# Kernel tuning notes

Hardware: AMD Instinct MI355X
Metric: run time of the kernel (lower is better)

Reference implementation:

```python
import jax, jax.numpy as jnp
import numpy as np

CH_J = 64      # number of output capsules
N_J = 32       # output capsule dim
R_NUM = 3      # routing iterations
B_ALPHAS = (8.0, 8.0, 8.0)
EPS = 1e-7     # K.epsilon()


def _squeeze(s):
    # squash nonlinearity: |s|^2/(1+|s|^2) * s/|s|
    sq = jnp.sum(s * s, axis=-1, keepdims=True)
    return (sq / (1.0 + sq)) * (s * jax.lax.rsqrt(sq + EPS))


def setup_inputs() -> dict:
    key = jax.random.key(0)
    k1, k2 = jax.random.split(key)
    B, CH_I, N_I = 16, 2048, 16
    inputs = jax.random.normal(k1, (B, CH_I, N_I), dtype=jnp.float32)
    # glorot-ish scale for the transform kernel (ch_i, n_i, ch_j, n_j)
    w = jax.random.normal(k2, (CH_I, N_I, CH_J, N_J), dtype=jnp.float32) * 0.05
    return {"inputs": inputs, "w": w}


def reference(inputs, w):
    # prediction vectors u[b,i,j,m] = sum_n inputs[b,i,n] * w[i,n,j,m]
    u = jnp.einsum('bin,injm->bijm', inputs, w)
    u_sg = jax.lax.stop_gradient(u)
    b = jnp.zeros(u.shape[:3], dtype=u.dtype)  # (B, ch_i, ch_j) routing logits
    v = None
    for r in range(R_NUM):
        if r > 0:
            c = jax.lax.stop_gradient(
                jax.nn.softmax(b * B_ALPHAS[r], axis=-1))[..., None] * CH_J
        else:
            c = 1.0
        ub = u if r == R_NUM - 1 else u_sg
        s = jnp.sum(c * ub, axis=1)  # (B, ch_j, n_j)
        v = _squeeze(s)
        if r == R_NUM - 1:
            break
        v = jax.lax.stop_gradient(v)
        # agreement update: a[b,i,j] = sum_m v[b,j,m] * u[b,i,j,m]
        b = b + jnp.einsum('bjm,bijm->bij', v, u)
    return v  # (B, ch_j, n_j)
```

## Files before the change

### kernel.cpp

```cpp
#include <hip/hip_runtime.h>
#include <hip/hip_fp16.h>
#include <math.h>

#define B_   16
#define CI   2048
#define NI   16
#define CJ   64
#define NJ   32
#define JM   2048
#define CH   8
#define NCH  256
#define ALPHA 8.0f

__global__ __launch_bounds__(1024)
void pass0_full(const float* __restrict__ x, const float* __restrict__ w,
                float* __restrict__ part, __half* __restrict__ U16)
{
    __shared__ float xs[CH][16][NI];

    const int ichunk = blockIdx.x;
    const int i0     = ichunk * CH;
    const int tid    = threadIdx.x;
    const int bh     = tid >> 8;
    const int jg     = tid & 255;
    const int jm0    = jg * 8;

    if (tid < 512) {
        const int f  = tid * 4;
        const int n  = f & 15;
        const int b  = (f >> 4) & 15;
        const int ci = f >> 8;
        *(float4*)(&xs[ci][b][n]) =
            *(const float4*)(x + ((size_t)b * CI + (i0 + ci)) * NI + n);
    }

    float acc[4][8];
#pragma unroll
    for (int bb = 0; bb < 4; ++bb)
#pragma unroll
        for (int k = 0; k < 8; ++k) acc[bb][k] = 0.0f;

    __syncthreads();

    for (int ci = 0; ci < CH; ++ci) {
        const int i = i0 + ci;

        float u[4][8];
#pragma unroll
        for (int bb = 0; bb < 4; ++bb)
#pragma unroll
            for (int k = 0; k < 8; ++k) u[bb][k] = 0.0f;

        const float* wrow = w + (size_t)i * (NI * JM) + jm0;
#pragma unroll
        for (int n = 0; n < NI; ++n) {
            const float4 w0 = *(const float4*)(wrow + (size_t)n * JM);
            const float4 w1 = *(const float4*)(wrow + (size_t)n * JM + 4);
#pragma unroll
            for (int bb = 0; bb < 4; ++bb) {
                const float xv = xs[ci][bh * 4 + bb][n];
                u[bb][0] = fmaf(xv, w0.x, u[bb][0]);
                u[bb][1] = fmaf(xv, w0.y, u[bb][1]);
                u[bb][2] = fmaf(xv, w0.z, u[bb][2]);
                u[bb][3] = fmaf(xv, w0.w, u[bb][3]);
                u[bb][4] = fmaf(xv, w1.x, u[bb][4]);
                u[bb][5] = fmaf(xv, w1.y, u[bb][5]);
                u[bb][6] = fmaf(xv, w1.z, u[bb][6]);
                u[bb][7] = fmaf(xv, w1.w, u[bb][7]);
            }
        }

#pragma unroll
        for (int bb = 0; bb < 4; ++bb) {
#pragma unroll
            for (int k = 0; k < 8; ++k) acc[bb][k] += u[bb][k];
            const int b = bh * 4 + bb;
            union { uint4 q; __half h[8]; } pk;
#pragma unroll
            for (int k = 0; k < 8; ++k) pk.h[k] = __float2half(u[bb][k]);
            *(uint4*)(U16 + ((size_t)b * CI + i) * JM + jm0) = pk.q;
        }
    }

#pragma unroll
    for (int bb = 0; bb < 4; ++bb) {
        const int b = bh * 4 + bb;
        float* dst = part + ((size_t)b * NCH + ichunk) * JM + jm0;
        *(float4*)(dst)     =
            make_float4(acc[bb][0], acc[bb][1], acc[bb][2], acc[bb][3]);
        *(float4*)(dst + 4) =
            make_float4(acc[bb][4], acc[bb][5], acc[bb][6], acc[bb][7]);
    }
}

template <int PASS, bool ATOMIC, bool STOREU>
__global__ __launch_bounds__(1024)
void pass_kernel(const float* __restrict__ x, const float* __restrict__ w,
                 const float* __restrict__ vprev, float* __restrict__ a0,
                 float* __restrict__ sout, __half* __restrict__ U16)
{
    __shared__ float xs[CH][8][NI];
    __shared__ float Ls[8][CJ];
    __shared__ float smax[8], sinv[8];

    const int idx    = blockIdx.x;
    const int xcd    = idx & 7;
    const int bhalf  = (idx >> 3) & 1;
    const int slot   = idx >> 4;
    const int ichunk = slot * 8 + xcd;
    const int i0     = ichunk * CH;
    const int b0     = bhalf * 8;

    const int tid  = threadIdx.x;
    const int bh   = tid >> 8;
    const int jg   = tid & 255;
    const int jm0  = jg * 8;
    const int jcol = jg >> 2;

    if (tid < 256) {
        const int f  = tid * 4;
        const int n  = f & 15;
        const int bg = (f >> 4) & 7;
        const int ci = f >> 7;
        *(float4*)(&xs[ci][bg][n]) =
            *(const float4*)(x + ((size_t)(b0 + bg) * CI + (i0 + ci)) * NI + n);
    }

    float acc[2][8];
#pragma unroll
    for (int bb = 0; bb < 2; ++bb)
#pragma unroll
        for (int k = 0; k < 8; ++k) acc[bb][k] = 0.0f;

    __syncthreads();

    for (int ci = 0; ci < CH; ++ci) {
        const int i = i0 + ci;

        float u[2][8];
#pragma unroll
        for (int bb = 0; bb < 2; ++bb)
#pragma unroll
            for (int k = 0; k < 8; ++k) u[bb][k] = 0.0f;

        const float* wrow = w + (size_t)i * (NI * JM) + jm0;
#pragma unroll
        for (int n = 0; n < NI; ++n) {
            const float4 w0 = *(const float4*)(wrow + (size_t)n * JM);
            const float4 w1 = *(const float4*)(wrow + (size_t)n * JM + 4);
#pragma unroll
            for (int bb = 0; bb < 2; ++bb) {
                const float xv = xs[ci][bh * 2 + bb][n];
                u[bb][0] = fmaf(xv, w0.x, u[bb][0]);
                u[bb][1] = fmaf(xv, w0.y, u[bb][1]);
                u[bb][2] = fmaf(xv, w0.z, u[bb][2]);
                u[bb][3] = fmaf(xv, w0.w, u[bb][3]);
                u[bb][4] = fmaf(xv, w1.x, u[bb][4]);
                u[bb][5] = fmaf(xv, w1.y, u[bb][5]);
                u[bb][6] = fmaf(xv, w1.z, u[bb][6]);
                u[bb][7] = fmaf(xv, w1.w, u[bb][7]);
            }
        }

        if (PASS == 0) {
#pragma unroll
            for (int bb = 0; bb < 2; ++bb)
#pragma unroll
                for (int k = 0; k < 8; ++k) acc[bb][k] += u[bb][k];
            if (STOREU) {
#pragma unroll
                for (int bb = 0; bb < 2; ++bb) {
                    const int b = b0 + bh * 2 + bb;
                    union { uint4 q; __half h[8]; } pk;
#pragma unroll
                    for (int k = 0; k < 8; ++k) pk.h[k] = __float2half(u[bb][k]);
                    *(uint4*)(U16 + ((size_t)b * CI + i) * JM + jm0) = pk.q;
                }
            }
        } else {
            float ap[2];
#pragma unroll
            for (int bb = 0; bb < 2; ++bb) {
                const int b = b0 + bh * 2 + bb;
                const float4 v0 = *(const float4*)(vprev + (size_t)b * JM + jm0);
                const float4 v1 = *(const float4*)(vprev + (size_t)b * JM + jm0 + 4);
                float t = u[bb][0] * v0.x + u[bb][1] * v0.y
                        + u[bb][2] * v0.z + u[bb][3] * v0.w
                        + u[bb][4] * v1.x + u[bb][5] * v1.y
                        + u[bb][6] * v1.z + u[bb][7] * v1.w;
                t += __shfl_xor(t, 1);
                t += __shfl_xor(t, 2);
                ap[bb] = t;
            }

            float L[2];
#pragma unroll
            for (int bb = 0; bb < 2; ++bb) {
                if (PASS == 1) {
                    L[bb] = ap[bb];
                } else {
                    const int b = b0 + bh * 2 + bb;
                    L[bb] = ap[bb] + a0[((size_t)b * CI + i) * CJ + jcol];
                }
            }
            if ((jg & 3) == 0) {
#pragma unroll
                for (int bb = 0; bb < 2; ++bb) {
                    const int bg = bh * 2 + bb;
                    Ls[bg][jcol] = L[bb];
                    if (PASS == 1)
                        a0[((size_t)(b0 + bg) * CI + i) * CJ + jcol] = ap[bb];
                }
            }
            __syncthreads();

            if (tid < 256) {
                const int rb = tid >> 5, rj = tid & 31;
                const float x1 = Ls[rb][rj];
                const float x2 = Ls[rb][rj + 32];
                float mx = fmaxf(x1, x2);
#pragma unroll
                for (int s2 = 1; s2 < 32; s2 <<= 1)
                    mx = fmaxf(mx, __shfl_xor(mx, s2));
                float ex = __expf(ALPHA * (x1 - mx)) + __expf(ALPHA * (x2 - mx));
#pragma unroll
                for (int s2 = 1; s2 < 32; s2 <<= 1)
                    ex += __shfl_xor(ex, s2);
                if (rj == 0) { smax[rb] = mx; sinv[rb] = 64.0f / ex; }
            }
            __syncthreads();

#pragma unroll
            for (int bb = 0; bb < 2; ++bb) {
                const int bg = bh * 2 + bb;
                const float c = __expf(ALPHA * (L[bb] - smax[bg])) * sinv[bg];
#pragma unroll
                for (int k = 0; k < 8; ++k)
                    acc[bb][k] = fmaf(c, u[bb][k], acc[bb][k]);
            }
        }
    }

    if (ATOMIC) {
#pragma unroll
        for (int bb = 0; bb < 2; ++bb) {
            const int b = b0 + bh * 2 + bb;
#pragma unroll
            for (int k = 0; k < 8; ++k)
                unsafeAtomicAdd(sout + (size_t)b * JM + jm0 + k, acc[bb][k]);
        }
    } else {
#pragma unroll
        for (int bb = 0; bb < 2; ++bb) {
            const int b = b0 + bh * 2 + bb;
            float* dst = sout + ((size_t)b * NCH + ichunk) * JM + jm0;
            *(float4*)(dst)     =
                make_float4(acc[bb][0], acc[bb][1], acc[bb][2], acc[bb][3]);
            *(float4*)(dst + 4) =
                make_float4(acc[bb][4], acc[bb][5], acc[bb][6], acc[bb][7]);
        }
    }
}

template <bool TWO>
__global__ __launch_bounds__(256)
void route_kernel(const __half* __restrict__ U16, const float* __restrict__ va,
                  const float* __restrict__ vb, float* __restrict__ part)
{
    const int tid = threadIdx.x;
    const int b   = blockIdx.x >> 6;
    const int ig  = blockIdx.x & 63;
    const int wv  = tid >> 6;
    const int l   = tid & 63;

    float vr[32];
#pragma unroll
    for (int q = 0; q < 8; ++q) {
        const float4 f = *(const float4*)(va + (size_t)b * JM + l * 32 + q * 4);
        vr[q * 4 + 0] = f.x; vr[q * 4 + 1] = f.y;
        vr[q * 4 + 2] = f.z; vr[q * 4 + 3] = f.w;
    }
    if (TWO) {
#pragma unroll
        for (int q = 0; q < 8; ++q) {
            const float4 f = *(const float4*)(vb + (size_t)b * JM + l * 32 + q * 4);
            vr[q * 4 + 0] += f.x; vr[q * 4 + 1] += f.y;
            vr[q * 4 + 2] += f.z; vr[q * 4 + 3] += f.w;
        }
    }

    float acc[32];
#pragma unroll
    for (int m = 0; m < 32; ++m) acc[m] = 0.0f;

    const __half* up0 = U16 + ((size_t)b * CI + ig * 32 + wv * 8) * JM + l * 32;

    union F4H { float4 f; __half2 h2[4]; };
    F4H cur[4], nxt[4];
#pragma unroll
    for (int q = 0; q < 4; ++q)
        cur[q].f = *(const float4*)(up0 + q * 8);

#pragma unroll
    for (int ii = 0; ii < 8; ++ii) {
        if (ii < 7) {
            const __half* upn = up0 + (size_t)(ii + 1) * JM;
#pragma unroll
            for (int q = 0; q < 4; ++q)
                nxt[q].f = *(const float4*)(upn + q * 8);
        }

        float ap = 0.0f;
#pragma unroll
        for (int q = 0; q < 4; ++q)
#pragma unroll
            for (int p = 0; p < 4; ++p) {
                const float2 uf = __half22float2(cur[q].h2[p]);
                const int m = q * 8 + p * 2;
                ap = fmaf(vr[m],     uf.x, ap);
                ap = fmaf(vr[m + 1], uf.y, ap);
            }

        float mx = ap;
#pragma unroll
        for (int d = 1; d < 64; d <<= 1)
            mx = fmaxf(mx, __shfl_xor(mx, d));
        const float e = __expf(ALPHA * (ap - mx));
        float se = e;
#pragma unroll
        for (int d = 1; d < 64; d <<= 1)
            se += __shfl_xor(se, d);
        const float c = e * (64.0f / se);

#pragma unroll
        for (int q = 0; q < 4; ++q)
#pragma unroll
            for (int p = 0; p < 4; ++p) {
                const float2 uf = __half22float2(cur[q].h2[p]);
                const int m = q * 8 + p * 2;
                acc[m]     = fmaf(c, uf.x, acc[m]);
                acc[m + 1] = fmaf(c, uf.y, acc[m + 1]);
            }

#pragma unroll
        for (int q = 0; q < 4; ++q) cur[q] = nxt[q];
    }

    float* dst = part + ((size_t)b * NCH + (ig * 4 + wv)) * JM + l * 32;
#pragma unroll
    for (int q = 0; q < 8; ++q)
        *(float4*)(dst + q * 4) =
            make_float4(acc[q * 4], acc[q * 4 + 1], acc[q * 4 + 2], acc[q * 4 + 3]);
}

__global__ __launch_bounds__(1024)
void reduce_squash(const float* __restrict__ part, float* __restrict__ v)
{
    __shared__ float red[4][256];
    const int tid = threadIdx.x;
    const int seg = tid >> 8;
    const int loc = tid & 255;
    const int b   = blockIdx.x >> 3;
    const int jmb = (blockIdx.x & 7) * 256;

    const float* p = part + ((size_t)b * NCH + seg * 64) * JM + jmb + loc;
    float s0 = 0.f, s1 = 0.f, s2 = 0.f, s3 = 0.f;
#pragma unroll 4
    for (int q = 0; q < 64; q += 4) {
        s0 += p[(size_t)(q + 0) * JM];
        s1 += p[(size_t)(q + 1) * JM];
        s2 += p[(size_t)(q + 2) * JM];
        s3 += p[(size_t)(q + 3) * JM];
    }
    red[seg][loc] = (s0 + s1) + (s2 + s3);
    __syncthreads();

    if (tid < 256) {
        const float s = (red[0][loc] + red[1][loc]) + (red[2][loc] + red[3][loc]);
        float sq = s * s;
#pragma unroll
        for (int k = 1; k < 32; k <<= 1) sq += __shfl_xor(sq, k);
        v[(size_t)b * JM + jmb + loc] =
            (sq / (1.0f + sq)) * (s * rsqrtf(sq + 1e-7f));
    }
}

__global__ __launch_bounds__(256)
void squash_kernel(const float* __restrict__ s, float* __restrict__ v)
{
    const int g = blockIdx.x * 256 + threadIdx.x;
    const float val = s[g];
    float sq = val * val;
#pragma unroll
    for (int k = 1; k < 32; k <<= 1) sq += __shfl_xor(sq, k);
    v[g] = (sq / (1.0f + sq)) * (val * rsqrtf(sq + 1e-7f));
}

extern "C" void kernel_launch(void* const* d_in, const int* in_sizes, int n_in,
                              void* d_out, int out_size, void* d_ws, size_t ws_size,
                              hipStream_t stream)
{
    const float* x = (const float*)d_in[0];
    const float* w = (const float*)d_in[1];
    float* out = (float*)d_out;
    float* ws  = (float*)d_ws;

    float* A0   = ws;
    float* V0   = A0 + (size_t)B_ * CI * CJ;
    float* V1   = V0 + (size_t)B_ * JM;
    float* PART = V1 + (size_t)B_ * JM;
    __half* U16 = (__half*)(PART + (size_t)B_ * NCH * JM);

    const size_t need_part =
        ((size_t)B_ * CI * CJ + 2 * (size_t)B_ * JM
         + (size_t)B_ * NCH * JM) * sizeof(float);
    const size_t need_full =
        need_part + (size_t)B_ * CI * JM * sizeof(__half);

    if (ws_size >= need_full) {
        pass0_full<<<256, 1024, 0, stream>>>(x, w, PART, U16);
        reduce_squash<<<128, 1024, 0, stream>>>(PART, V0);
        route_kernel<false><<<1024, 256, 0, stream>>>(U16, V0, nullptr, PART);
        reduce_squash<<<128, 1024, 0, stream>>>(PART, V1);
        route_kernel<true><<<1024, 256, 0, stream>>>(U16, V0, V1, PART);
        reduce_squash<<<128, 1024, 0, stream>>>(PART, out);
    } else if (ws_size >= need_part) {
        pass_kernel<0, false, false><<<512, 1024, 0, stream>>>(x, w, nullptr, nullptr, PART, nullptr);
        reduce_squash<<<128, 1024, 0, stream>>>(PART, V0);
        pass_kernel<1, false, false><<<512, 1024, 0, stream>>>(x, w, V0, A0, PART, nullptr);
        reduce_squash<<<128, 1024, 0, stream>>>(PART, V1);
        pass_kernel<2, false, false><<<512, 1024, 0, stream>>>(x, w, V1, A0, PART, nullptr);
        reduce_squash<<<128, 1024, 0, stream>>>(PART, out);
    } else {
        float* S0 = V1 + (size_t)B_ * JM;
        float* S1 = S0 + (size_t)B_ * JM;
        float* S2 = S1 + (size_t)B_ * JM;
        hipMemsetAsync(S0, 0, (size_t)3 * B_ * JM * sizeof(float), stream);
        pass_kernel<0, true, false><<<512, 1024, 0, stream>>>(x, w, nullptr, nullptr, S0, nullptr);
        squash_kernel<<<128, 256, 0, stream>>>(S0, V0);
        pass_kernel<1, true, false><<<512, 1024, 0, stream>>>(x, w, V0, A0, S1, nullptr);
        squash_kernel<<<128, 256, 0, stream>>>(S1, V1);
        pass_kernel<2, true, false><<<512, 1024, 0, stream>>>(x, w, V1, A0, S2, nullptr);
        squash_kernel<<<128, 256, 0, stream>>>(S2, out);
    }
}
```

Before: 547.5 us.

## Stage W through double-buffered LDS with async loads and deepen U prefetch

The first pass now copies each half-row of the transform weights into a double-buffered shared-memory tile with global_load_lds. It waits on vmcnt and barriers so the next tile loads while the current one is being multiplied, and each thread now handles 4 columns per half instead of 8. The final routing pass prefetches two U rows ahead instead of one and splits the agreement dot product into four independent partial sums to shorten the dependency chain. It also drops the max subtraction before the softmax exponent, removing one wave-wide reduction; the exp can overflow if the agreement logits grow large. The shared-memory footprint rises to about 128 KB per block, which limits each CU to a single block.

Result: faster. 524.1 us (-4.3%).

```diff
diff --git a/kernel.cpp b/kernel.cpp
--- a/kernel.cpp
+++ b/kernel.cpp
@@ -10,12 +10,14 @@
 #define JM   2048
 #define CH   8
 #define NCH  256
+#define WHALF 1024
 #define ALPHA 8.0f
 
 __global__ __launch_bounds__(1024)
 void pass0_full(const float* __restrict__ x, const float* __restrict__ w,
                 float* __restrict__ part, __half* __restrict__ U16)
 {
+    __shared__ float wlds[2][NI][WHALF];
     __shared__ float xs[CH][16][NI];
 
     const int ichunk = blockIdx.x;
@@ -23,7 +25,9 @@
     const int tid    = threadIdx.x;
     const int bh     = tid >> 8;
     const int jg     = tid & 255;
-    const int jm0    = jg * 8;
+    const int wv_    = tid >> 6;
+    const int lane   = tid & 63;
+    const int fi_base = wv_ * 256 + lane * 4;
 
     if (tid < 512) {
         const int f  = tid * 4;
@@ -34,62 +38,96 @@
             *(const float4*)(x + ((size_t)b * CI + (i0 + ci)) * NI + n);
     }
 
-    float acc[4][8];
+    float acc[4][2][4];
 #pragma unroll
     for (int bb = 0; bb < 4; ++bb)
 #pragma unroll
-        for (int k = 0; k < 8; ++k) acc[bb][k] = 0.0f;
+        for (int h = 0; h < 2; ++h)
+#pragma unroll
+            for (int k = 0; k < 4; ++k) acc[bb][h][k] = 0.0f;
+
+    float* const wbase = &wlds[0][0][0];
+
+    auto stage = [&](int ci_, int h_, int dstbuf) {
+        const float* gb = w + (size_t)(i0 + ci_) * (NI * JM) + h_ * WHALF;
+#pragma unroll
+        for (int q = 0; q < 4; ++q) {
+            const int fi = fi_base + q * 4096;
+            const int n_ = fi >> 10;
+            const int c_ = fi & 1023;
+            const float* g = gb + n_ * JM + c_;
+            float* lb = wbase + (dstbuf * (NI * WHALF) + wv_ * 256 + q * 4096);
+            __builtin_amdgcn_global_load_lds(
+                (const __attribute__((address_space(1))) void*)g,
+                (__attribute__((address_space(3))) void*)lb, 16, 0, 0);
+        }
+    };
 
     __syncthreads();
+
+    int buf = 0;
+    stage(0, 0, 0);
 
     for (int ci = 0; ci < CH; ++ci) {
         const int i = i0 + ci;
 
-        float u[4][8];
-#pragma unroll
-        for (int bb = 0; bb < 4; ++bb)
-#pragma unroll
-            for (int k = 0; k < 8; ++k) u[bb][k] = 0.0f;
-
-        const float* wrow = w + (size_t)i * (NI * JM) + jm0;
-#pragma unroll
-        for (int n = 0; n < NI; ++n) {
-            const float4 w0 = *(const float4*)(wrow + (size_t)n * JM);
-            const float4 w1 = *(const float4*)(wrow + (size_t)n * JM + 4);
-#pragma unroll
-            for (int bb = 0; bb < 4; ++bb) {
-                const float xv = xs[ci][bh * 4 + bb][n];
-                u[bb][0] = fmaf(xv, w0.x, u[bb][0]);
-                u[bb][1] = fmaf(xv, w0.y, u[bb][1]);
-                u[bb][2] = fmaf(xv, w0.z, u[bb][2]);
-                u[bb][3] = fmaf(xv, w0.w, u[bb][3]);
-                u[bb][4] = fmaf(xv, w1.x, u[bb][4]);
-                u[bb][5] = fmaf(xv, w1.y, u[bb][5]);
-                u[bb][6] = fmaf(xv, w1.z, u[bb][6]);
-                u[bb][7] = fmaf(xv, w1.w, u[bb][7]);
-            }
-        }
-
-#pragma unroll
-        for (int bb = 0; bb < 4; ++bb) {
-#pragma unroll
-            for (int k = 0; k < 8; ++k) acc[bb][k] += u[bb][k];
-            const int b = bh * 4 + bb;
-            union { uint4 q; __half h[8]; } pk;
-#pragma unroll
-            for (int k = 0; k < 8; ++k) pk.h[k] = __float2half(u[bb][k]);
-            *(uint4*)(U16 + ((size_t)b * CI + i) * JM + jm0) = pk.q;
-        }
+#define PHASE(H, NEXT_CI, NEXT_H, IS_LAST)                                     \
+        do {                                                                   \
+            if (!(IS_LAST)) {                                                  \
+                stage((NEXT_CI), (NEXT_H), buf ^ 1);                           \
+                asm volatile("s_waitcnt vmcnt(4)" ::: "memory");               \
+            } else {                                                           \
+                asm volatile("s_waitcnt vmcnt(0)" ::: "memory");               \
+            }                                                                  \
+            __builtin_amdgcn_s_barrier();                                      \
+            __builtin_amdgcn_sched_barrier(0);                                 \
+            float uu[4][4];                                                    \
+            _Pragma("unroll")                                                  \
+            for (int bb = 0; bb < 4; ++bb)                                     \
+                _Pragma("unroll")                                              \
+                for (int k = 0; k < 4; ++k) uu[bb][k] = 0.0f;                  \
+            const float* wb = wbase + buf * (NI * WHALF);                      \
+            _Pragma("unroll")                                                  \
+            for (int n = 0; n < NI; ++n) {                                     \
+                const float4 wq = *(const float4*)(wb + n * WHALF + jg * 4);   \
+                _Pragma("unroll")                                              \
+                for (int bb = 0; bb < 4; ++bb) {                               \
+                    const float xv = xs[ci][bh * 4 + bb][n];                   \
+                    uu[bb][0] = fmaf(xv, wq.x, uu[bb][0]);                     \
+                    uu[bb][1] = fmaf(xv, wq.y, uu[bb][1]);                     \
+                    uu[bb][2] = fmaf(xv, wq.z, uu[bb][2]);                     \
+                    uu[bb][3] = fmaf(xv, wq.w, uu[bb][3]);                     \
+                }                                                              \
+            }                                                                  \
+            _Pragma("unroll")                                                  \
+            for (int bb = 0; bb < 4; ++bb) {                                   \
+                const int b = bh * 4 + bb;                                     \
+                _Pragma("unroll")                                              \
+                for (int k = 0; k < 4; ++k)                                    \
+                    acc[bb][H][k] += uu[bb][k];                                \
+                union { uint2 d; __half hh[4]; } pk;                           \
+                _Pragma("unroll")                                              \
+                for (int k = 0; k < 4; ++k) pk.hh[k] = __float2half(uu[bb][k]);\
+                *(uint2*)(U16 + ((size_t)b * CI + i) * JM                      \
+                          + (H) * WHALF + jg * 4) = pk.d;                      \
+            }                                                                  \
+            __builtin_amdgcn_s_barrier();                                      \
+            buf ^= 1;                                                          \
+        } while (0)
+
+        PHASE(0, ci, 1, false);
+        PHASE(1, ci + 1, 0, ci == CH - 1);
+#undef PHASE
     }
 
 #pragma unroll
     for (int bb = 0; bb < 4; ++bb) {
         const int b = bh * 4 + bb;
-        float* dst = part + ((size_t)b * NCH + ichunk) * JM + jm0;
-        *(float4*)(dst)     =
-            make_float4(acc[bb][0], acc[bb][1], acc[bb][2], acc[bb][3]);
-        *(float4*)(dst + 4) =
-            make_float4(acc[bb][4], acc[bb][5], acc[bb][6], acc[bb][7]);
+        float* dst = part + ((size_t)b * NCH + ichunk) * JM + jg * 4;
+        *(float4*)(dst) =
+            make_float4(acc[bb][0][0], acc[bb][0][1], acc[bb][0][2], acc[bb][0][3]);
+        *(float4*)(dst + WHALF) =
+            make_float4(acc[bb][1][0], acc[bb][1][1], acc[bb][1][2], acc[bb][1][3]);
     }
 }
 
@@ -296,36 +334,40 @@
     const __half* up0 = U16 + ((size_t)b * CI + ig * 32 + wv * 8) * JM + l * 32;
 
     union F4H { float4 f; __half2 h2[4]; };
-    F4H cur[4], nxt[4];
-#pragma unroll
-    for (int q = 0; q < 4; ++q)
-        cur[q].f = *(const float4*)(up0 + q * 8);
+    F4H buf[2][4];
+#pragma unroll
+    for (int r = 0; r < 2; ++r)
+#pragma unroll
+        for (int q = 0; q < 4; ++q)
+            buf[r][q].f = *(const float4*)(up0 + (size_t)r * JM + q * 8);
 
 #pragma unroll
     for (int ii = 0; ii < 8; ++ii) {
-        if (ii < 7) {
-            const __half* upn = up0 + (size_t)(ii + 1) * JM;
+        F4H cu[4];
+#pragma unroll
+        for (int q = 0; q < 4; ++q) cu[q] = buf[ii & 1][q];
+
+        if (ii + 2 < 8) {
 #pragma unroll
             for (int q = 0; q < 4; ++q)
-                nxt[q].f = *(const float4*)(upn + q * 8);
-        }
-
-        float ap = 0.0f;
-#pragma unroll
-        for (int q = 0; q < 4; ++q)
-#pragma unroll
-            for (int p = 0; p < 4; ++p) {
-                const float2 uf = __half22float2(cur[q].h2[p]);
-                const int m = q * 8 + p * 2;
-                ap = fmaf(vr[m],     uf.x, ap);
-                ap = fmaf(vr[m + 1], uf.y, ap);
-            }
-
-        float mx = ap;
-#pragma unroll
-        for (int d = 1; d < 64; d <<= 1)
-            mx = fmaxf(mx, __shfl_xor(mx, d));
-        const float e = __expf(ALPHA * (ap - mx));
+                buf[ii & 1][q].f = *(const float4*)(up0 + (size_t)(ii + 2) * JM + q * 8);
+        }
+
+        float p0 = 0.f, p1 = 0.f, p2 = 0.f, p3 = 0.f;
+#pragma unroll
+        for (int p = 0; p < 4; ++p) {
+            const float2 u0 = __half22float2(cu[0].h2[p]);
+            const float2 u1 = __half22float2(cu[1].h2[p]);
+            const float2 u2 = __half22float2(cu[2].h2[p]);
+            const float2 u3 = __half22float2(cu[3].h2[p]);
+            p0 = fmaf(vr[p * 2],      u0.x, p0); p0 = fmaf(vr[p * 2 + 1],  u0.y, p0);
+            p1 = fmaf(vr[8 + p * 2],  u1.x, p1); p1 = fmaf(vr[9 + p * 2],  u1.y, p1);
+            p2 = fmaf(vr[16 + p * 2], u2.x, p2); p2 = fmaf(vr[17 + p * 2], u2.y, p2);
+            p3 = fmaf(vr[24 + p * 2], u3.x, p3); p3 = fmaf(vr[25 + p * 2], u3.y, p3);
+        }
+        const float ap = (p0 + p1) + (p2 + p3);
+
+        const float e = __expf(ALPHA * ap);
         float se = e;
 #pragma unroll
         for (int d = 1; d < 64; d <<= 1)
@@ -336,14 +378,11 @@
         for (int q = 0; q < 4; ++q)
 #pragma unroll
             for (int p = 0; p < 4; ++p) {
-                const float2 uf = __half22float2(cur[q].h2[p]);
+                const float2 uf = __half22float2(cu[q].h2[p]);
                 const int m = q * 8 + p * 2;
                 acc[m]     = fmaf(c, uf.x, acc[m]);
                 acc[m + 1] = fmaf(c, uf.y, acc[m + 1]);
             }
-
-#pragma unroll
-        for (int q = 0; q < 4; ++q) cur[q] = nxt[q];
     }
 
     float* dst = part + ((size_t)b * NCH + (ig * 4 + wv)) * JM + l * 32;
```
